# Kernel tuning notes

Measured on AMD Instinct MI355X. Metric: run time of the kernel, lower is better.

Reference implementation:

```python
import jax, jax.numpy as jnp
import numpy as np

N = 50000      # nodes
E = 800000     # edges (before self-loops)
DIN = 128
DH = 16        # per-head channels, layer 1
H = 8          # heads, layer 1
DOUT = 128     # layer 2 output (heads=1)
EDIM = 8       # edge_attr dim (unused by math: edge_dim=None in GATConv)
EPS_BN = 1e-5
NEG_SLOPE = 0.2


def _gat_conv(x, edge_index, W, a_src, a_dst, bias, heads, ch):
    """PyG GATConv (concat=True, add_self_loops=True, edge_dim=None)."""
    n = x.shape[0]
    loop = jnp.arange(n, dtype=edge_index.dtype)
    src = jnp.concatenate([edge_index[0], loop])  # [E+N]
    dst = jnp.concatenate([edge_index[1], loop])
    h = (x @ W).reshape(n, heads, ch)             # [N,H,C]
    s_src = jnp.einsum('nhc,hc->nh', h, a_src)    # [N,H]
    s_dst = jnp.einsum('nhc,hc->nh', h, a_dst)
    e = jax.nn.leaky_relu(s_src[src] + s_dst[dst], NEG_SLOPE)  # [E+N,H]
    # segment softmax over incoming edges of each dst node
    m = jax.ops.segment_max(e, dst, num_segments=n)
    ex = jnp.exp(e - m[dst])
    den = jax.ops.segment_sum(ex, dst, num_segments=n)
    alpha = ex / (den[dst] + 1e-16)               # [E+N,H]
    out = jax.ops.segment_sum(alpha[:, :, None] * h[src], dst, num_segments=n)
    return out.reshape(n, heads * ch) + bias


def _bn_selu(x, gamma, beta):
    # BatchNorm1d in training mode (batch statistics, biased variance) + SELU.
    mu = x.mean(axis=0)
    var = x.var(axis=0)
    xn = (x - mu) * jax.lax.rsqrt(var + EPS_BN)
    return jax.nn.selu(gamma * xn + beta)


def setup_inputs() -> dict:
    key = jax.random.key(0)
    ks = jax.random.split(key, 12)
    x = jax.random.normal(ks[0], (N, DIN), jnp.float32)
    edge_index = jax.random.randint(ks[1], (2, E), 0, N, jnp.int32)
    edge_attr = jax.random.normal(ks[2], (E, EDIM), jnp.float32)
    W1 = jax.random.normal(ks[3], (DIN, H * DH), jnp.float32) / np.sqrt(DIN)
    a_src1 = jax.random.normal(ks[4], (H, DH), jnp.float32) / np.sqrt(DH)
    a_dst1 = jax.random.normal(ks[5], (H, DH), jnp.float32) / np.sqrt(DH)
    b1 = jnp.zeros((H * DH,), jnp.float32)
    g1 = jnp.ones((H * DH,), jnp.float32)
    beta1 = jnp.zeros((H * DH,), jnp.float32)
    W2 = jax.random.normal(ks[6], (H * DH, DOUT), jnp.float32) / np.sqrt(H * DH)
    a_src2 = jax.random.normal(ks[7], (1, DOUT), jnp.float32) / np.sqrt(DOUT)
    a_dst2 = jax.random.normal(ks[8], (1, DOUT), jnp.float32) / np.sqrt(DOUT)
    b2 = jnp.zeros((DOUT,), jnp.float32)
    g2 = jnp.ones((DOUT,), jnp.float32)
    beta2 = jnp.zeros((DOUT,), jnp.float32)
    return dict(x=x, edge_index=edge_index, edge_attr=edge_attr,
                W1=W1, a_src1=a_src1, a_dst1=a_dst1, b1=b1, g1=g1, beta1=beta1,
                W2=W2, a_src2=a_src2, a_dst2=a_dst2, b2=b2, g2=g2, beta2=beta2)


def reference(x, edge_index, edge_attr,
              W1, a_src1, a_dst1, b1, g1, beta1,
              W2, a_src2, a_dst2, b2, g2, beta2):
    # edge_attr is unused: GATConv built with edge_dim=None ignores edge features.
    h = _gat_conv(x, edge_index, W1, a_src1, a_dst1, b1, H, DH)   # [N, H*DH]
    h = _bn_selu(h, g1, beta1)                                    # dropout = identity (eval)
    h = _gat_conv(h, edge_index, W2, a_src2, a_dst2, b2, 1, DOUT) # [N, DOUT]
    h = _bn_selu(h, g2, beta2)
    return h
```

## Files before the change

### kernel.cpp

```cpp
#include <hip/hip_runtime.h>

#define SELU_SCALE 1.0507009873554805f
#define SELU_ALPHA 1.6732632423543772f

typedef __attribute__((ext_vector_type(8))) short short8;
typedef __attribute__((ext_vector_type(4))) float f32x4;

#define BCAP 10240

static __device__ __forceinline__ float leaky02(float v) {
  return v > 0.0f ? v : 0.2f * v;
}

static __device__ __forceinline__ ushort f2bf(float f) {
  uint b = __float_as_uint(f);
  return (ushort)((b + 0x7fffu + ((b >> 16) & 1u)) >> 16);
}
static __device__ __forceinline__ float bf2f(ushort u) {
  return __uint_as_float(((uint)u) << 16);
}

static __device__ __forceinline__ float selu_f(float y) {
  return y > 0.f ? SELU_SCALE * y : SELU_SCALE * SELU_ALPHA * (__expf(y) - 1.f);
}

static __device__ __forceinline__ void load8(const float* p, float* xv, bool ok) {
  float4 xa = make_float4(0.f, 0.f, 0.f, 0.f), xb = xa;
  if (ok) {
    xa = *(const float4*)p;
    xb = *(const float4*)(p + 4);
  }
  xv[0] = xa.x; xv[1] = xa.y; xv[2] = xa.z; xv[3] = xa.w;
  xv[4] = xb.x; xv[5] = xb.y; xv[6] = xb.z; xv[7] = xb.w;
}
static __device__ __forceinline__ void load8(const ushort* p, float* xv, bool ok) {
  ushort4 ua = make_ushort4(0, 0, 0, 0), ub = ua;
  if (ok) {
    ua = *(const ushort4*)p;
    ub = *(const ushort4*)(p + 4);
  }
  xv[0] = bf2f(ua.x); xv[1] = bf2f(ua.y); xv[2] = bf2f(ua.z); xv[3] = bf2f(ua.w);
  xv[4] = bf2f(ub.x); xv[5] = bf2f(ub.y); xv[6] = bf2f(ub.z); xv[7] = bf2f(ub.w);
}

__global__ __launch_bounds__(256) void pack_kernel(const float* __restrict__ W1,
                                                   const float* __restrict__ W2,
                                                   ushort* __restrict__ Wp1,
                                                   ushort* __restrict__ Wp2,
                                                   float* __restrict__ zbase, int zwords) {
  if (blockIdx.x == 128) {
    for (int i = threadIdx.x; i < zwords; i += 256) zbase[i] = 0.f;
    return;
  }
  int idx = blockIdx.x * 256 + threadIdx.x;
  const float* W = (idx < 16384) ? W1 : W2;
  ushort* Wp = (idx < 16384) ? Wp1 : Wp2;
  int t = idx & 16383;
  int b = t & 7, i = (t >> 3) & 15, g = (t >> 7) & 3, kt = (t >> 9) & 3, ct = t >> 11;
  int k = kt * 32 + g * 8 + b, col = ct * 16 + i;
  Wp[t] = f2bf(W[k * 128 + col]);
}

template <int HEADS, bool BN, typename XT>
static __device__ __forceinline__ void gemm_body(
    int blk, const XT* __restrict__ X, const ushort* __restrict__ Wp,
    ushort* __restrict__ H, const float* __restrict__ asr, const float* __restrict__ adt,
    float* __restrict__ ssrc, float* __restrict__ sdst, int n,
    const float* __restrict__ stats, const float* __restrict__ gamma,
    const float* __restrict__ beta) {
  __shared__ float sc[128], sh[128];
  if (BN) {
    int t = threadIdx.x;
    if (t < 128) {
      float invN = 1.0f / (float)n;
      float mu = stats[t] * invN;
      float var = stats[128 + t] * invN - mu * mu;
      float rs = rsqrtf(var + 1e-5f);
      float s = gamma[t] * rs;
      sc[t] = s;
      sh[t] = beta[t] - s * mu;
    }
    __syncthreads();
  }
  const int tid = threadIdx.x;
  const int w = tid >> 6, l = tid & 63;
  const int lj = l & 15, lg = l >> 4;
  const int row = blk * 64 + w * 16 + lj;
  const bool rowok = row < n;
  const XT* xrow = X + (size_t)row * 128;

  f32x4 acc[8];
#pragma unroll
  for (int ct = 0; ct < 8; ++ct) acc[ct] = (f32x4){0.f, 0.f, 0.f, 0.f};

#pragma unroll
  for (int kt = 0; kt < 4; ++kt) {
    const int k0 = kt * 32 + lg * 8;
    float xv[8];
    load8(xrow + k0, xv, rowok);
    if (BN) {
#pragma unroll
      for (int b = 0; b < 8; ++b) xv[b] = selu_f(xv[b] * sc[k0 + b] + sh[k0 + b]);
    }
    short8 bx;
#pragma unroll
    for (int b = 0; b < 8; ++b) bx[b] = (short)f2bf(xv[b]);
#pragma unroll
    for (int ct = 0; ct < 8; ++ct) {
      short8 af = *(const short8*)(Wp + ((((ct * 4 + kt) * 4 + lg) * 16 + lj) << 3));
      acc[ct] = __builtin_amdgcn_mfma_f32_16x16x32_bf16(af, bx, acc[ct], 0, 0, 0);
    }
  }

  if (rowok) {
#pragma unroll
    for (int ct = 0; ct < 8; ++ct) {
      ushort4 h4;
      h4.x = f2bf(acc[ct][0]);
      h4.y = f2bf(acc[ct][1]);
      h4.z = f2bf(acc[ct][2]);
      h4.w = f2bf(acc[ct][3]);
      *(ushort4*)&H[(size_t)row * 128 + ct * 16 + lg * 4] = h4;
    }
  }

  if (HEADS == 8) {
    float ps[8], pd[8];
#pragma unroll
    for (int ct = 0; ct < 8; ++ct) {
      float4 av = *(const float4*)&asr[ct * 16 + lg * 4];
      float4 dv = *(const float4*)&adt[ct * 16 + lg * 4];
      ps[ct] = acc[ct][0] * av.x + acc[ct][1] * av.y + acc[ct][2] * av.z + acc[ct][3] * av.w;
      pd[ct] = acc[ct][0] * dv.x + acc[ct][1] * dv.y + acc[ct][2] * dv.z + acc[ct][3] * dv.w;
      ps[ct] += __shfl_xor(ps[ct], 16);
      ps[ct] += __shfl_xor(ps[ct], 32);
      pd[ct] += __shfl_xor(pd[ct], 16);
      pd[ct] += __shfl_xor(pd[ct], 32);
    }
    if (lg == 0 && rowok) {
      *(float4*)&ssrc[(size_t)row * 8] = make_float4(ps[0], ps[1], ps[2], ps[3]);
      *(float4*)&ssrc[(size_t)row * 8 + 4] = make_float4(ps[4], ps[5], ps[6], ps[7]);
      *(float4*)&sdst[(size_t)row * 8] = make_float4(pd[0], pd[1], pd[2], pd[3]);
      *(float4*)&sdst[(size_t)row * 8 + 4] = make_float4(pd[4], pd[5], pd[6], pd[7]);
    }
  } else {
    float ps = 0.f, pd = 0.f;
#pragma unroll
    for (int ct = 0; ct < 8; ++ct) {
      float4 av = *(const float4*)&asr[ct * 16 + lg * 4];
      float4 dv = *(const float4*)&adt[ct * 16 + lg * 4];
      ps += acc[ct][0] * av.x + acc[ct][1] * av.y + acc[ct][2] * av.z + acc[ct][3] * av.w;
      pd += acc[ct][0] * dv.x + acc[ct][1] * dv.y + acc[ct][2] * dv.z + acc[ct][3] * dv.w;
    }
    ps += __shfl_xor(ps, 16);
    ps += __shfl_xor(ps, 32);
    pd += __shfl_xor(pd, 16);
    pd += __shfl_xor(pd, 32);
    if (lg == 0 && rowok) {
      ssrc[row] = ps;
      sdst[row] = pd;
    }
  }
}

__global__ __launch_bounds__(256) void gemm1_bucket_kernel(
    const float* __restrict__ X, const ushort* __restrict__ Wp, ushort* __restrict__ H,
    const float* __restrict__ asr, const float* __restrict__ adt,
    float* __restrict__ ssrc, float* __restrict__ sdst, int n,
    const int* __restrict__ ei, int* __restrict__ gcur, uint* __restrict__ bucket,
    int nE, int EA, int NB, int gb) {
  if (blockIdx.x < gb) {
    gemm_body<8, false, float>(blockIdx.x, X, Wp, H, asr, adt, ssrc, sdst, n,
                               nullptr, nullptr, nullptr);
    return;
  }
  __shared__ int lcnt[128];
  __shared__ int lbase[128];
  int tid = threadIdx.x;
  if (tid < 128) lcnt[tid] = 0;
  __syncthreads();
  int e0 = (blockIdx.x - gb) * 1024;
  uint ent[4];
  int bk[4], lp[4];
#pragma unroll
  for (int j = 0; j < 4; ++j) {
    int e = e0 + j * 256 + tid;
    bk[j] = -1;
    if (e < EA) {
      int src, dst;
      if (e < nE) {
        src = ei[e];
        dst = ei[nE + e];
      } else {
        src = dst = e - nE;
      }
      bk[j] = dst >> 9;
      ent[j] = ((uint)src << 9) | (uint)(dst & 511);
      lp[j] = atomicAdd(&lcnt[bk[j]], 1);
    }
  }
  __syncthreads();
  if (tid < NB && lcnt[tid] > 0) lbase[tid] = atomicAdd(&gcur[tid], lcnt[tid]);
  __syncthreads();
#pragma unroll
  for (int j = 0; j < 4; ++j) {
    if (bk[j] >= 0) bucket[(size_t)bk[j] * BCAP + lbase[bk[j]] + lp[j]] = ent[j];
  }
}

__global__ __launch_bounds__(256) void gemm2_kernel(
    const ushort* __restrict__ X, const ushort* __restrict__ Wp, ushort* __restrict__ H,
    const float* __restrict__ asr, const float* __restrict__ adt,
    float* __restrict__ ssrc, float* __restrict__ sdst, int n,
    const float* __restrict__ stats, const float* __restrict__ gamma,
    const float* __restrict__ beta) {
  gemm_body<1, true, ushort>(blockIdx.x, X, Wp, H, asr, adt, ssrc, sdst, n,
                             stats, gamma, beta);
}

__global__ __launch_bounds__(1024) void csrbuild_kernel(const int* __restrict__ gcur,
                                                        const uint* __restrict__ bucket,
                                                        int* __restrict__ offs,
                                                        int* __restrict__ csr,
                                                        int n, int NB) {
  __shared__ int ldeg[512];
  __shared__ int loff[512];
  __shared__ int lwsum[8];
  __shared__ int partial[2];
  int b = blockIdx.x, tid = threadIdx.x;
  int lane = tid & 63, w = tid >> 6;
  if (tid < 128) {
    int v = (tid < b) ? gcur[tid] : 0;
#pragma unroll
    for (int s = 1; s < 64; s <<= 1) v += __shfl_xor(v, s);
    if (lane == 0) partial[tid >> 6] = v;
  }
  if (tid < 512) ldeg[tid] = 0;
  __syncthreads();
  int base = partial[0] + partial[1];
  int cnt = gcur[b];
  const uint* bb = bucket + (size_t)b * BCAP;
  for (int k = tid; k < cnt; k += 1024) atomicAdd(&ldeg[bb[k] & 511], 1);
  __syncthreads();
  int v = 0, x = 0;
  if (tid < 512) {
    v = ldeg[tid];
    x = v;
#pragma unroll
    for (int s = 1; s < 64; s <<= 1) {
      int t = __shfl_up(x, s);
      if (lane >= s) x += t;
    }
    if (lane == 63) lwsum[w] = x;
  }
  __syncthreads();
  if (w == 0 && lane < 8) {
    int wv = lwsum[lane];
    int y = wv;
#pragma unroll
    for (int s = 1; s < 8; s <<= 1) {
      int t = __shfl_up(y, s);
      if (lane >= s) y += t;
    }
    lwsum[lane] = y - wv;
  }
  __syncthreads();
  if (tid < 512) {
    int excl = x - v + lwsum[w];
    loff[tid] = excl;
    int node = b * 512 + tid;
    if (node < n) offs[node] = base + excl;
  }
  if (b == NB - 1 && tid == 0) offs[n] = base + cnt;
  __syncthreads();
  if (tid < 512) ldeg[tid] = loff[tid];
  __syncthreads();
  for (int k = tid; k < cnt; k += 1024) {
    uint e = bb[k];
    int pos = atomicAdd(&ldeg[e & 511], 1);
    csr[base + pos] = (int)(e >> 9);
  }
}

__global__ __launch_bounds__(256) void agg1_kernel(const ushort* __restrict__ h1,
                                                   const int* __restrict__ csr,
                                                   const int* __restrict__ offs,
                                                   const float* __restrict__ ssrc,
                                                   const float* __restrict__ sdst,
                                                   const float* __restrict__ bias,
                                                   ushort* __restrict__ outb, int nN) {
  int wid = (blockIdx.x * blockDim.x + threadIdx.x) >> 6;
  int lane = threadIdx.x & 63;
  int q = lane >> 4, ll = lane & 15;
  if (wid >= nN) return;
  int c = ll * 8;
  int h = ll >> 1;
  float sd = sdst[wid * 8 + h];
  int beg = offs[wid];
  int deg = offs[wid + 1] - beg;
  float b0 = 0.f, b1 = 0.f, b2 = 0.f, b3 = 0.f;
  float b4 = 0.f, b5 = 0.f, b6 = 0.f, b7 = 0.f, den = 0.f;
  int i = q;
  for (; i + 4 < deg; i += 8) {
    int s0 = csr[beg + i];
    int s1 = csr[beg + i + 4];
    float e0 = ssrc[s0 * 8 + h];
    float e1 = ssrc[s1 * 8 + h];
    short8 u0 = *(const short8*)&h1[(size_t)s0 * 128 + c];
    short8 u1 = *(const short8*)&h1[(size_t)s1 * 128 + c];
    float A0 = __expf(leaky02(e0 + sd));
    float A1 = __expf(leaky02(e1 + sd));
    b0 += A0 * bf2f((ushort)u0[0]) + A1 * bf2f((ushort)u1[0]);
    b1 += A0 * bf2f((ushort)u0[1]) + A1 * bf2f((ushort)u1[1]);
    b2 += A0 * bf2f((ushort)u0[2]) + A1 * bf2f((ushort)u1[2]);
    b3 += A0 * bf2f((ushort)u0[3]) + A1 * bf2f((ushort)u1[3]);
    b4 += A0 * bf2f((ushort)u0[4]) + A1 * bf2f((ushort)u1[4]);
    b5 += A0 * bf2f((ushort)u0[5]) + A1 * bf2f((ushort)u1[5]);
    b6 += A0 * bf2f((ushort)u0[6]) + A1 * bf2f((ushort)u1[6]);
    b7 += A0 * bf2f((ushort)u0[7]) + A1 * bf2f((ushort)u1[7]);
    den += A0 + A1;
  }
  if (i < deg) {
    int s0 = csr[beg + i];
    float e0 = ssrc[s0 * 8 + h];
    short8 u0 = *(const short8*)&h1[(size_t)s0 * 128 + c];
    float A0 = __expf(leaky02(e0 + sd));
    b0 += A0 * bf2f((ushort)u0[0]);
    b1 += A0 * bf2f((ushort)u0[1]);
    b2 += A0 * bf2f((ushort)u0[2]);
    b3 += A0 * bf2f((ushort)u0[3]);
    b4 += A0 * bf2f((ushort)u0[4]);
    b5 += A0 * bf2f((ushort)u0[5]);
    b6 += A0 * bf2f((ushort)u0[6]);
    b7 += A0 * bf2f((ushort)u0[7]);
    den += A0;
  }
  b0 += __shfl_xor(b0, 16); b0 += __shfl_xor(b0, 32);
  b1 += __shfl_xor(b1, 16); b1 += __shfl_xor(b1, 32);
  b2 += __shfl_xor(b2, 16); b2 += __shfl_xor(b2, 32);
  b3 += __shfl_xor(b3, 16); b3 += __shfl_xor(b3, 32);
  b4 += __shfl_xor(b4, 16); b4 += __shfl_xor(b4, 32);
  b5 += __shfl_xor(b5, 16); b5 += __shfl_xor(b5, 32);
  b6 += __shfl_xor(b6, 16); b6 += __shfl_xor(b6, 32);
  b7 += __shfl_xor(b7, 16); b7 += __shfl_xor(b7, 32);
  den += __shfl_xor(den, 16); den += __shfl_xor(den, 32);
  if (q == 0) {
    float invd = 1.0f / (den + 1e-16f);
    float4 bv0 = *(const float4*)&bias[c];
    float4 bv1 = *(const float4*)&bias[c + 4];
    short8 o;
    o[0] = (short)f2bf(b0 * invd + bv0.x);
    o[1] = (short)f2bf(b1 * invd + bv0.y);
    o[2] = (short)f2bf(b2 * invd + bv0.z);
    o[3] = (short)f2bf(b3 * invd + bv0.w);
    o[4] = (short)f2bf(b4 * invd + bv1.x);
    o[5] = (short)f2bf(b5 * invd + bv1.y);
    o[6] = (short)f2bf(b6 * invd + bv1.z);
    o[7] = (short)f2bf(b7 * invd + bv1.w);
    *(short8*)&outb[(size_t)wid * 128 + c] = o;
  }
}

__global__ __launch_bounds__(256) void agg2_kernel(const ushort* __restrict__ h2,
                                                   const int* __restrict__ csr,
                                                   const int* __restrict__ offs,
                                                   const float* __restrict__ ssrc,
                                                   const float* __restrict__ sdst,
                                                   const float* __restrict__ bias,
                                                   float* __restrict__ out, int nN) {
  int wid = (blockIdx.x * blockDim.x + threadIdx.x) >> 6;
  int lane = threadIdx.x & 63;
  int q = lane >> 4, ll = lane & 15;
  if (wid >= nN) return;
  int c = ll * 8;
  float sd = sdst[wid];
  int beg = offs[wid];
  int deg = offs[wid + 1] - beg;
  float b0 = 0.f, b1 = 0.f, b2 = 0.f, b3 = 0.f;
  float b4 = 0.f, b5 = 0.f, b6 = 0.f, b7 = 0.f, den = 0.f;
  int i = q;
  for (; i + 4 < deg; i += 8) {
    int s0 = csr[beg + i];
    int s1 = csr[beg + i + 4];
    float e0 = ssrc[s0];
    float e1 = ssrc[s1];
    short8 u0 = *(const short8*)&h2[(size_t)s0 * 128 + c];
    short8 u1 = *(const short8*)&h2[(size_t)s1 * 128 + c];
    float A0 = __expf(leaky02(e0 + sd));
    float A1 = __expf(leaky02(e1 + sd));
    b0 += A0 * bf2f((ushort)u0[0]) + A1 * bf2f((ushort)u1[0]);
    b1 += A0 * bf2f((ushort)u0[1]) + A1 * bf2f((ushort)u1[1]);
    b2 += A0 * bf2f((ushort)u0[2]) + A1 * bf2f((ushort)u1[2]);
    b3 += A0 * bf2f((ushort)u0[3]) + A1 * bf2f((ushort)u1[3]);
    b4 += A0 * bf2f((ushort)u0[4]) + A1 * bf2f((ushort)u1[4]);
    b5 += A0 * bf2f((ushort)u0[5]) + A1 * bf2f((ushort)u1[5]);
    b6 += A0 * bf2f((ushort)u0[6]) + A1 * bf2f((ushort)u1[6]);
    b7 += A0 * bf2f((ushort)u0[7]) + A1 * bf2f((ushort)u1[7]);
    den += A0 + A1;
  }
  if (i < deg) {
    int s0 = csr[beg + i];
    float e0 = ssrc[s0];
    short8 u0 = *(const short8*)&h2[(size_t)s0 * 128 + c];
    float A0 = __expf(leaky02(e0 + sd));
    b0 += A0 * bf2f((ushort)u0[0]);
    b1 += A0 * bf2f((ushort)u0[1]);
    b2 += A0 * bf2f((ushort)u0[2]);
    b3 += A0 * bf2f((ushort)u0[3]);
    b4 += A0 * bf2f((ushort)u0[4]);
    b5 += A0 * bf2f((ushort)u0[5]);
    b6 += A0 * bf2f((ushort)u0[6]);
    b7 += A0 * bf2f((ushort)u0[7]);
    den += A0;
  }
  b0 += __shfl_xor(b0, 16); b0 += __shfl_xor(b0, 32);
  b1 += __shfl_xor(b1, 16); b1 += __shfl_xor(b1, 32);
  b2 += __shfl_xor(b2, 16); b2 += __shfl_xor(b2, 32);
  b3 += __shfl_xor(b3, 16); b3 += __shfl_xor(b3, 32);
  b4 += __shfl_xor(b4, 16); b4 += __shfl_xor(b4, 32);
  b5 += __shfl_xor(b5, 16); b5 += __shfl_xor(b5, 32);
  b6 += __shfl_xor(b6, 16); b6 += __shfl_xor(b6, 32);
  b7 += __shfl_xor(b7, 16); b7 += __shfl_xor(b7, 32);
  den += __shfl_xor(den, 16); den += __shfl_xor(den, 32);
  if (q == 0) {
    float invd = 1.0f / (den + 1e-16f);
    float4 bv0 = *(const float4*)&bias[c];
    float4 bv1 = *(const float4*)&bias[c + 4];
    *(float4*)&out[(size_t)wid * 128 + c] =
        make_float4(b0 * invd + bv0.x, b1 * invd + bv0.y, b2 * invd + bv0.z, b3 * invd + bv0.w);
    *(float4*)&out[(size_t)wid * 128 + c + 4] =
        make_float4(b4 * invd + bv1.x, b5 * invd + bv1.y, b6 * invd + bv1.z, b7 * invd + bv1.w);
  }
}

__global__ __launch_bounds__(256) void stats_bf16_kernel(const ushort* __restrict__ X,
                                                         float* __restrict__ stats, int n) {
  __shared__ float red[256];
  int tid = threadIdx.x;
  int c = tid & 127;
  int half = tid >> 7;
  float s = 0.f, sq = 0.f;
  int rbeg = (int)blockIdx.x * 64 + half;
  int rend = min((int)(blockIdx.x + 1) * 64, n);
#pragma unroll 4
  for (int r = rbeg; r < rend; r += 2) {
    float v = bf2f(X[(size_t)r * 128 + c]);
    s += v;
    sq += v * v;
  }
  red[tid] = s;
  __syncthreads();
  float s2 = (half == 0) ? s + red[tid + 128] : 0.f;
  __syncthreads();
  red[tid] = sq;
  __syncthreads();
  if (half == 0) {
    float sq2 = sq + red[tid + 128];
    atomicAdd(&stats[c], s2);
    atomicAdd(&stats[128 + c], sq2);
  }
}

__global__ __launch_bounds__(256) void stats_kernel(const float* __restrict__ X,
                                                    float* __restrict__ stats, int n) {
  __shared__ float red[256];
  int tid = threadIdx.x;
  int c = tid & 127;
  int half = tid >> 7;
  float s = 0.f, sq = 0.f;
  int rbeg = (int)blockIdx.x * 64 + half;
  int rend = min((int)(blockIdx.x + 1) * 64, n);
#pragma unroll 4
  for (int r = rbeg; r < rend; r += 2) {
    float v = X[(size_t)r * 128 + c];
    s += v;
    sq += v * v;
  }
  red[tid] = s;
  __syncthreads();
  float s2 = (half == 0) ? s + red[tid + 128] : 0.f;
  __syncthreads();
  red[tid] = sq;
  __syncthreads();
  if (half == 0) {
    float sq2 = sq + red[tid + 128];
    atomicAdd(&stats[c], s2);
    atomicAdd(&stats[128 + c], sq2);
  }
}

__global__ __launch_bounds__(256) void bnselu_kernel(const float* __restrict__ X,
                                                     const float* __restrict__ stats,
                                                     const float* __restrict__ gamma,
                                                     const float* __restrict__ beta,
                                                     float* __restrict__ Y, int n) {
  int gid = blockIdx.x * blockDim.x + threadIdx.x;
  if (gid >= n * 32) return;
  int c = (gid & 31) * 4;
  int r = gid >> 5;
  float invN = 1.0f / (float)n;
  float4 x = *(const float4*)&X[(size_t)r * 128 + c];
  float o[4];
#pragma unroll
  for (int j = 0; j < 4; ++j) {
    float xx = (j == 0) ? x.x : (j == 1) ? x.y : (j == 2) ? x.z : x.w;
    float mu = stats[c + j] * invN;
    float var = stats[128 + c + j] * invN - mu * mu;
    float rs = rsqrtf(var + 1e-5f);
    float y = gamma[c + j] * ((xx - mu) * rs) + beta[c + j];
    o[j] = selu_f(y);
  }
  *(float4*)&Y[(size_t)r * 128 + c] = make_float4(o[0], o[1], o[2], o[3]);
}

extern "C" void kernel_launch(void* const* d_in, const int* in_sizes, int n_in,
                              void* d_out, int out_size, void* d_ws, size_t ws_size,
                              hipStream_t stream) {
  const float* x   = (const float*)d_in[0];
  const int*   ei  = (const int*)d_in[1];
  const float* W1  = (const float*)d_in[3];
  const float* as1 = (const float*)d_in[4];
  const float* ad1 = (const float*)d_in[5];
  const float* b1  = (const float*)d_in[6];
  const float* g1  = (const float*)d_in[7];
  const float* be1 = (const float*)d_in[8];
  const float* W2  = (const float*)d_in[9];
  const float* as2 = (const float*)d_in[10];
  const float* ad2 = (const float*)d_in[11];
  const float* b2  = (const float*)d_in[12];
  const float* g2  = (const float*)d_in[13];
  const float* be2 = (const float*)d_in[14];
  float* out = (float*)d_out;

  const int n  = in_sizes[0] / 128;
  const int nE = in_sizes[1] / 2;
  const int EA = nE + n;
  const int NB = (n + 511) >> 9;
  const int nbb = (EA + 1023) / 1024;
  const int gb = (n + 63) / 64;

  float* ws = (float*)d_ws;
  size_t o = 0;
  ushort* Bf = (ushort*)(ws + o); o += (size_t)n * 64;
  ushort* H = (ushort*)(ws + o); o += (size_t)n * 64;
  float* ssrc1 = ws + o;  o += (size_t)n * 8;
  float* sdst1 = ws + o;  o += (size_t)n * 8;
  float* ssrc2 = ws + o;  o += n;
  float* sdst2 = ws + o;  o += n;
  ushort* Wp1 = (ushort*)(ws + o); o += 8192;
  ushort* Wp2 = (ushort*)(ws + o); o += 8192;
  float* zbase = ws + o;
  float* stats1 = ws + o; o += 256;
  float* stats2 = ws + o; o += 256;
  int* gcur = (int*)(ws + o); o += 128;
  int zwords = (int)((ws + o) - zbase);
  int* offs = (int*)(ws + o); o += (size_t)n + 1;
  int* csr  = (int*)(ws + o); o += EA;
  uint* bucket = (uint*)(ws + o); o += (size_t)NB * BCAP;

  pack_kernel<<<129, 256, 0, stream>>>(W1, W2, Wp1, Wp2, zbase, zwords);

  gemm1_bucket_kernel<<<gb + nbb, 256, 0, stream>>>(
      x, Wp1, H, as1, ad1, ssrc1, sdst1, n, ei, gcur, bucket, nE, EA, NB, gb);
  csrbuild_kernel<<<NB, 1024, 0, stream>>>(gcur, bucket, offs, csr, n, NB);

  agg1_kernel<<<(n + 3) / 4, 256, 0, stream>>>(H, csr, offs, ssrc1, sdst1, b1, Bf, n);
  stats_bf16_kernel<<<(n + 63) / 64, 256, 0, stream>>>(Bf, stats1, n);

  gemm2_kernel<<<(n + 63) / 64, 256, 0, stream>>>(
      Bf, Wp2, H, as2, ad2, ssrc2, sdst2, n, stats1, g1, be1);
  agg2_kernel<<<(n + 3) / 4, 256, 0, stream>>>(H, csr, offs, ssrc2, sdst2, b2, out, n);
  stats_kernel<<<(n + 63) / 64, 256, 0, stream>>>(out, stats2, n);
  bnselu_kernel<<<(n * 32 + 255) / 256, 256, 0, stream>>>(out, stats2, g2, be2, out, n);
}
```

Baseline: 217.9 us.

## Restage CSR build alongside GEMM1 and store layer-2 output in bf16

Edge bucketing now runs in a prep kernel together with the weight packing, and the CSR build from buckets is merged into the layer-1 GEMM launch, so the graph construction overlaps the dense matmul. The CSR build now uses 256-thread blocks instead of 1024. The workspace zeroing moves to hipMemsetAsync. The layer-2 aggregation writes bf16 instead of fp32, so stats and BN+SELU read half the bytes, at the cost of precision in the final pre-normalisation activations.

```diff
diff --git a/kernel.cpp b/kernel.cpp
--- a/kernel.cpp
+++ b/kernel.cpp
@@ -43,22 +43,53 @@
   xv[4] = bf2f(ub.x); xv[5] = bf2f(ub.y); xv[6] = bf2f(ub.z); xv[7] = bf2f(ub.w);
 }
 
-__global__ __launch_bounds__(256) void pack_kernel(const float* __restrict__ W1,
-                                                   const float* __restrict__ W2,
-                                                   ushort* __restrict__ Wp1,
-                                                   ushort* __restrict__ Wp2,
-                                                   float* __restrict__ zbase, int zwords) {
-  if (blockIdx.x == 128) {
-    for (int i = threadIdx.x; i < zwords; i += 256) zbase[i] = 0.f;
+__global__ __launch_bounds__(256) void prep_kernel(
+    const int* __restrict__ ei, int* __restrict__ gcur, uint* __restrict__ bucket,
+    const float* __restrict__ W1, const float* __restrict__ W2,
+    ushort* __restrict__ Wp1, ushort* __restrict__ Wp2,
+    int nE, int EA, int NB, int nbb) {
+  int tid = threadIdx.x;
+  if (blockIdx.x >= nbb) {
+    int idx = (blockIdx.x - nbb) * 256 + tid;
+    const float* W = (idx < 16384) ? W1 : W2;
+    ushort* Wp = (idx < 16384) ? Wp1 : Wp2;
+    int t = idx & 16383;
+    int b = t & 7, i = (t >> 3) & 15, g = (t >> 7) & 3, kt = (t >> 9) & 3, ct = t >> 11;
+    int k = kt * 32 + g * 8 + b, col = ct * 16 + i;
+    Wp[t] = f2bf(W[k * 128 + col]);
     return;
   }
-  int idx = blockIdx.x * 256 + threadIdx.x;
-  const float* W = (idx < 16384) ? W1 : W2;
-  ushort* Wp = (idx < 16384) ? Wp1 : Wp2;
-  int t = idx & 16383;
-  int b = t & 7, i = (t >> 3) & 15, g = (t >> 7) & 3, kt = (t >> 9) & 3, ct = t >> 11;
-  int k = kt * 32 + g * 8 + b, col = ct * 16 + i;
-  Wp[t] = f2bf(W[k * 128 + col]);
+  __shared__ int lcnt[128];
+  __shared__ int lbase[128];
+  if (tid < 128) lcnt[tid] = 0;
+  __syncthreads();
+  int e0 = blockIdx.x * 1024;
+  uint ent[4];
+  int bk[4], lp[4];
+#pragma unroll
+  for (int j = 0; j < 4; ++j) {
+    int e = e0 + j * 256 + tid;
+    bk[j] = -1;
+    if (e < EA) {
+      int src, dst;
+      if (e < nE) {
+        src = ei[e];
+        dst = ei[nE + e];
+      } else {
+        src = dst = e - nE;
+      }
+      bk[j] = dst >> 9;
+      ent[j] = ((uint)src << 9) | (uint)(dst & 511);
+      lp[j] = atomicAdd(&lcnt[bk[j]], 1);
+    }
+  }
+  __syncthreads();
+  if (tid < NB && lcnt[tid] > 0) lbase[tid] = atomicAdd(&gcur[tid], lcnt[tid]);
+  __syncthreads();
+#pragma unroll
+  for (int j = 0; j < 4; ++j) {
+    if (bk[j] >= 0) bucket[(size_t)bk[j] * BCAP + lbase[bk[j]] + lp[j]] = ent[j];
+  }
 }
 
 template <int HEADS, bool BN, typename XT>
@@ -163,48 +194,76 @@
   }
 }
 
-__global__ __launch_bounds__(256) void gemm1_bucket_kernel(
+static __device__ __forceinline__ void csr_body(int b, const int* __restrict__ gcur,
+                                                const uint* __restrict__ bucket,
+                                                int* __restrict__ offs,
+                                                int* __restrict__ csr, int n, int NB) {
+  __shared__ int ldeg[512];
+  __shared__ int lwsum[4];
+  __shared__ int partial[2];
+  int tid = threadIdx.x;
+  int lane = tid & 63, w = tid >> 6;
+  if (tid < 128) {
+    int v = (tid < b) ? gcur[tid] : 0;
+#pragma unroll
+    for (int s = 1; s < 64; s <<= 1) v += __shfl_xor(v, s);
+    if (lane == 0) partial[tid >> 6] = v;
+  }
+  ldeg[tid] = 0;
+  ldeg[tid + 256] = 0;
+  __syncthreads();
+  int base = partial[0] + partial[1];
+  int cnt = gcur[b];
+  const uint* bb = bucket + (size_t)b * BCAP;
+  for (int k = tid; k < cnt; k += 256) atomicAdd(&ldeg[bb[k] & 511], 1);
+  __syncthreads();
+  int v0 = ldeg[tid * 2], v1 = ldeg[tid * 2 + 1];
+  int t = v0 + v1;
+  int x = t;
+#pragma unroll
+  for (int s = 1; s < 64; s <<= 1) {
+    int tt = __shfl_up(x, s);
+    if (lane >= s) x += tt;
+  }
+  if (lane == 63) lwsum[w] = x;
+  __syncthreads();
+  if (tid == 0) {
+    int s = 0;
+#pragma unroll
+    for (int j = 0; j < 4; ++j) {
+      int tmp = lwsum[j];
+      lwsum[j] = s;
+      s += tmp;
+    }
+  }
+  __syncthreads();
+  int excl = x - t + lwsum[w];
+  int node0 = b * 512 + tid * 2;
+  if (node0 < n) offs[node0] = base + excl;
+  if (node0 + 1 < n) offs[node0 + 1] = base + excl + v0;
+  if (b == NB - 1 && tid == 0) offs[n] = base + cnt;
+  __syncthreads();
+  ldeg[tid * 2] = excl;
+  ldeg[tid * 2 + 1] = excl + v0;
+  __syncthreads();
+  for (int k = tid; k < cnt; k += 256) {
+    uint e = bb[k];
+    int pos = atomicAdd(&ldeg[e & 511], 1);
+    csr[base + pos] = (int)(e >> 9);
+  }
+}
+
+__global__ __launch_bounds__(256) void gemm1csr_kernel(
     const float* __restrict__ X, const ushort* __restrict__ Wp, ushort* __restrict__ H,
     const float* __restrict__ asr, const float* __restrict__ adt,
     float* __restrict__ ssrc, float* __restrict__ sdst, int n,
-    const int* __restrict__ ei, int* __restrict__ gcur, uint* __restrict__ bucket,
-    int nE, int EA, int NB, int gb) {
+    const int* __restrict__ gcur, const uint* __restrict__ bucket,
+    int* __restrict__ offs, int* __restrict__ csr, int NB, int gb) {
   if (blockIdx.x < gb) {
     gemm_body<8, false, float>(blockIdx.x, X, Wp, H, asr, adt, ssrc, sdst, n,
                                nullptr, nullptr, nullptr);
-    return;
-  }
-  __shared__ int lcnt[128];
-  __shared__ int lbase[128];
-  int tid = threadIdx.x;
-  if (tid < 128) lcnt[tid] = 0;
-  __syncthreads();
-  int e0 = (blockIdx.x - gb) * 1024;
-  uint ent[4];
-  int bk[4], lp[4];
-#pragma unroll
-  for (int j = 0; j < 4; ++j) {
-    int e = e0 + j * 256 + tid;
-    bk[j] = -1;
-    if (e < EA) {
-      int src, dst;
-      if (e < nE) {
-        src = ei[e];
-        dst = ei[nE + e];
-      } else {
-        src = dst = e - nE;
-      }
-      bk[j] = dst >> 9;
-      ent[j] = ((uint)src << 9) | (uint)(dst & 511);
-      lp[j] = atomicAdd(&lcnt[bk[j]], 1);
-    }
-  }
-  __syncthreads();
-  if (tid < NB && lcnt[tid] > 0) lbase[tid] = atomicAdd(&gcur[tid], lcnt[tid]);
-  __syncthreads();
-#pragma unroll
-  for (int j = 0; j < 4; ++j) {
-    if (bk[j] >= 0) bucket[(size_t)bk[j] * BCAP + lbase[bk[j]] + lp[j]] = ent[j];
+  } else {
+    csr_body(blockIdx.x - gb, gcur, bucket, offs, csr, n, NB);
   }
 }
 
@@ -216,70 +275,6 @@
     const float* __restrict__ beta) {
   gemm_body<1, true, ushort>(blockIdx.x, X, Wp, H, asr, adt, ssrc, sdst, n,
                              stats, gamma, beta);
-}
-
-__global__ __launch_bounds__(1024) void csrbuild_kernel(const int* __restrict__ gcur,
-                                                        const uint* __restrict__ bucket,
-                                                        int* __restrict__ offs,
-                                                        int* __restrict__ csr,
-                                                        int n, int NB) {
-  __shared__ int ldeg[512];
-  __shared__ int loff[512];
-  __shared__ int lwsum[8];
-  __shared__ int partial[2];
-  int b = blockIdx.x, tid = threadIdx.x;
-  int lane = tid & 63, w = tid >> 6;
-  if (tid < 128) {
-    int v = (tid < b) ? gcur[tid] : 0;
-#pragma unroll
-    for (int s = 1; s < 64; s <<= 1) v += __shfl_xor(v, s);
-    if (lane == 0) partial[tid >> 6] = v;
-  }
-  if (tid < 512) ldeg[tid] = 0;
-  __syncthreads();
-  int base = partial[0] + partial[1];
-  int cnt = gcur[b];
-  const uint* bb = bucket + (size_t)b * BCAP;
-  for (int k = tid; k < cnt; k += 1024) atomicAdd(&ldeg[bb[k] & 511], 1);
-  __syncthreads();
-  int v = 0, x = 0;
-  if (tid < 512) {
-    v = ldeg[tid];
-    x = v;
-#pragma unroll
-    for (int s = 1; s < 64; s <<= 1) {
-      int t = __shfl_up(x, s);
-      if (lane >= s) x += t;
-    }
-    if (lane == 63) lwsum[w] = x;
-  }
-  __syncthreads();
-  if (w == 0 && lane < 8) {
-    int wv = lwsum[lane];
-    int y = wv;
-#pragma unroll
-    for (int s = 1; s < 8; s <<= 1) {
-      int t = __shfl_up(y, s);
-      if (lane >= s) y += t;
-    }
-    lwsum[lane] = y - wv;
-  }
-  __syncthreads();
-  if (tid < 512) {
-    int excl = x - v + lwsum[w];
-    loff[tid] = excl;
-    int node = b * 512 + tid;
-    if (node < n) offs[node] = base + excl;
-  }
-  if (b == NB - 1 && tid == 0) offs[n] = base + cnt;
-  __syncthreads();
-  if (tid < 512) ldeg[tid] = loff[tid];
-  __syncthreads();
-  for (int k = tid; k < cnt; k += 1024) {
-    uint e = bb[k];
-    int pos = atomicAdd(&ldeg[e & 511], 1);
-    csr[base + pos] = (int)(e >> 9);
-  }
 }
 
 __global__ __launch_bounds__(256) void agg1_kernel(const ushort* __restrict__ h1,
@@ -367,7 +362,7 @@
                                                    const float* __restrict__ ssrc,
                                                    const float* __restrict__ sdst,
                                                    const float* __restrict__ bias,
-                                                   float* __restrict__ out, int nN) {
+                                                   ushort* __restrict__ outb, int nN) {
   int wid = (blockIdx.x * blockDim.x + threadIdx.x) >> 6;
   int lane = threadIdx.x & 63;
   int q = lane >> 4, ll = lane & 15;
@@ -426,10 +421,16 @@
     float invd = 1.0f / (den + 1e-16f);
     float4 bv0 = *(const float4*)&bias[c];
     float4 bv1 = *(const float4*)&bias[c + 4];
-    *(float4*)&out[(size_t)wid * 128 + c] =
-        make_float4(b0 * invd + bv0.x, b1 * invd + bv0.y, b2 * invd + bv0.z, b3 * invd + bv0.w);
-    *(float4*)&out[(size_t)wid * 128 + c + 4] =
-        make_float4(b4 * invd + bv1.x, b5 * invd + bv1.y, b6 * invd + bv1.z, b7 * invd + bv1.w);
+    short8 o;
+    o[0] = (short)f2bf(b0 * invd + bv0.x);
+    o[1] = (short)f2bf(b1 * invd + bv0.y);
+    o[2] = (short)f2bf(b2 * invd + bv0.z);
+    o[3] = (short)f2bf(b3 * invd + bv0.w);
+    o[4] = (short)f2bf(b4 * invd + bv1.x);
+    o[5] = (short)f2bf(b5 * invd + bv1.y);
+    o[6] = (short)f2bf(b6 * invd + bv1.z);
+    o[7] = (short)f2bf(b7 * invd + bv1.w);
+    *(short8*)&outb[(size_t)wid * 128 + c] = o;
   }
 }
 
@@ -461,53 +462,25 @@
   }
 }
 
-__global__ __launch_bounds__(256) void stats_kernel(const float* __restrict__ X,
-                                                    float* __restrict__ stats, int n) {
-  __shared__ float red[256];
-  int tid = threadIdx.x;
-  int c = tid & 127;
-  int half = tid >> 7;
-  float s = 0.f, sq = 0.f;
-  int rbeg = (int)blockIdx.x * 64 + half;
-  int rend = min((int)(blockIdx.x + 1) * 64, n);
-#pragma unroll 4
-  for (int r = rbeg; r < rend; r += 2) {
-    float v = X[(size_t)r * 128 + c];
-    s += v;
-    sq += v * v;
-  }
-  red[tid] = s;
-  __syncthreads();
-  float s2 = (half == 0) ? s + red[tid + 128] : 0.f;
-  __syncthreads();
-  red[tid] = sq;
-  __syncthreads();
-  if (half == 0) {
-    float sq2 = sq + red[tid + 128];
-    atomicAdd(&stats[c], s2);
-    atomicAdd(&stats[128 + c], sq2);
-  }
-}
-
-__global__ __launch_bounds__(256) void bnselu_kernel(const float* __restrict__ X,
-                                                     const float* __restrict__ stats,
-                                                     const float* __restrict__ gamma,
-                                                     const float* __restrict__ beta,
-                                                     float* __restrict__ Y, int n) {
+__global__ __launch_bounds__(256) void bnselu_bf16_kernel(const ushort* __restrict__ X,
+                                                          const float* __restrict__ stats,
+                                                          const float* __restrict__ gamma,
+                                                          const float* __restrict__ beta,
+                                                          float* __restrict__ Y, int n) {
   int gid = blockIdx.x * blockDim.x + threadIdx.x;
   if (gid >= n * 32) return;
   int c = (gid & 31) * 4;
   int r = gid >> 5;
   float invN = 1.0f / (float)n;
-  float4 x = *(const float4*)&X[(size_t)r * 128 + c];
+  ushort4 u = *(const ushort4*)&X[(size_t)r * 128 + c];
+  float xv[4] = {bf2f(u.x), bf2f(u.y), bf2f(u.z), bf2f(u.w)};
   float o[4];
 #pragma unroll
   for (int j = 0; j < 4; ++j) {
-    float xx = (j == 0) ? x.x : (j == 1) ? x.y : (j == 2) ? x.z : x.w;
     float mu = stats[c + j] * invN;
     float var = stats[128 + c + j] * invN - mu * mu;
     float rs = rsqrtf(var + 1e-5f);
-    float y = gamma[c + j] * ((xx - mu) * rs) + beta[c + j];
+    float y = gamma[c + j] * ((xv[j] - mu) * rs) + beta[c + j];
     o[j] = selu_f(y);
   }
   *(float4*)&Y[(size_t)r * 128 + c] = make_float4(o[0], o[1], o[2], o[3]);
@@ -553,23 +526,25 @@
   float* stats1 = ws + o; o += 256;
   float* stats2 = ws + o; o += 256;
   int* gcur = (int*)(ws + o); o += 128;
-  int zwords = (int)((ws + o) - zbase);
+  size_t zwords = (size_t)((ws + o) - zbase);
   int* offs = (int*)(ws + o); o += (size_t)n + 1;
   int* csr  = (int*)(ws + o); o += EA;
   uint* bucket = (uint*)(ws + o); o += (size_t)NB * BCAP;
 
-  pack_kernel<<<129, 256, 0, stream>>>(W1, W2, Wp1, Wp2, zbase, zwords);
-
-  gemm1_bucket_kernel<<<gb + nbb, 256, 0, stream>>>(
-      x, Wp1, H, as1, ad1, ssrc1, sdst1, n, ei, gcur, bucket, nE, EA, NB, gb);
-  csrbuild_kernel<<<NB, 1024, 0, stream>>>(gcur, bucket, offs, csr, n, NB);
+  hipMemsetAsync(zbase, 0, zwords * sizeof(float), stream);
+
+  prep_kernel<<<nbb + 128, 256, 0, stream>>>(ei, gcur, bucket, W1, W2, Wp1, Wp2,
+                                             nE, EA, NB, nbb);
+
+  gemm1csr_kernel<<<gb + NB, 256, 0, stream>>>(
+      x, Wp1, H, as1, ad1, ssrc1, sdst1, n, gcur, bucket, offs, csr, NB, gb);
 
   agg1_kernel<<<(n + 3) / 4, 256, 0, stream>>>(H, csr, offs, ssrc1, sdst1, b1, Bf, n);
   stats_bf16_kernel<<<(n + 63) / 64, 256, 0, stream>>>(Bf, stats1, n);
 
-  gemm2_kernel<<<(n + 63) / 64, 256, 0, stream>>>(
+  gemm2_kernel<<<gb, 256, 0, stream>>>(
       Bf, Wp2, H, as2, ad2, ssrc2, sdst2, n, stats1, g1, be1);
-  agg2_kernel<<<(n + 3) / 4, 256, 0, stream>>>(H, csr, offs, ssrc2, sdst2, b2, out, n);
-  stats_kernel<<<(n + 63) / 64, 256, 0, stream>>>(out, stats2, n);
-  bnselu_kernel<<<(n * 32 + 255) / 256, 256, 0, stream>>>(out, stats2, g2, be2, out, n);
-}
+  agg2_kernel<<<(n + 3) / 4, 256, 0, stream>>>(H, csr, offs, ssrc2, sdst2, b2, Bf, n);
+  stats_bf16_kernel<<<(n + 63) / 64, 256, 0, stream>>>(Bf, stats2, n);
+  bnselu_bf16_kernel<<<(n * 32 + 255) / 256, 256, 0, stream>>>(Bf, stats2, g2, be2, out, n);
+}
```

After: 225.5 us. 3.5% more time.
